# Kernel optimization log

Measured on AMD Instinct MI355X. Metric: run time of the kernel, lower is better.

## Reference

```python
import jax, jax.numpy as jnp
import numpy as np
from jax import lax

EPS = 1e-5

def ste_sign(x):
    # forward-only module: plain sign is fine
    return jnp.sign(x)

def conv2d(x, w, pad):
    # x: NCHW, w: OIHW, stride 1
    return lax.conv_general_dilated(x, w, window_strides=(1, 1),
                                    padding=[(pad, pad), (pad, pad)],
                                    dimension_numbers=('NCHW', 'OIHW', 'NCHW'))

def maxpool2(x):
    # 2x2 max pool, stride 2, VALID (floor) -- matches nn.MaxPool2d(2,2)
    return lax.reduce_window(x, -jnp.inf, lax.max, (1, 1, 2, 2), (1, 1, 2, 2), 'VALID')

def batchnorm(x, gamma, beta):
    # training-mode BN: batch statistics over (N,H,W), biased variance
    mean = jnp.mean(x, axis=(0, 2, 3), keepdims=True)
    var = jnp.var(x, axis=(0, 2, 3), keepdims=True)
    xn = (x - mean) * lax.rsqrt(var + EPS)
    return xn * gamma[None, :, None, None] + beta[None, :, None, None]

def setup_inputs() -> dict:
    key = jax.random.key(0)
    ks = jax.random.split(key, 8)
    def he(k, shape):
        n = shape[2] * shape[3] * shape[0]
        return jax.random.normal(k, shape, jnp.float32) * np.sqrt(2.0 / n)
    x = jax.random.normal(ks[0], (4096, 1, 28, 28), jnp.float32)
    w0 = he(ks[1], (32, 1, 3, 3))
    w1 = he(ks[2], (32, 32, 3, 3))
    w2 = he(ks[3], (32, 32, 3, 3))
    g0 = jnp.ones((32,), jnp.float32); b0 = jnp.zeros((32,), jnp.float32)
    g1 = jnp.ones((32,), jnp.float32); b1 = jnp.zeros((32,), jnp.float32)
    g2 = jnp.ones((32,), jnp.float32); b2 = jnp.zeros((32,), jnp.float32)
    fw = jax.random.normal(ks[4], (10, 288), jnp.float32) * 0.01
    fb = jnp.zeros((10,), jnp.float32)
    return {"x": x, "w0": w0, "g0": g0, "b0": b0, "w1": w1, "g1": g1, "b1": b1,
            "w2": w2, "g2": g2, "b2": b2, "fw": fw, "fb": fb}

def reference(x, w0, g0, b0, w1, g1, b1, w2, g2, b2, fw, fb):
    # block0: fp conv -> pool -> bn (no act)
    h = batchnorm(maxpool2(conv2d(x, w0, 1)), g0, b0)          # [B,32,14,14]
    # block1: binary(1w1a) conv -> pool -> bn + maxpool(shortcut)
    o = batchnorm(maxpool2(conv2d(ste_sign(h), ste_sign(w1), 1)), g1, b1)
    h = o + maxpool2(h)                                         # [B,32,7,7]
    # block2
    o = batchnorm(maxpool2(conv2d(ste_sign(h), ste_sign(w2), 1)), g2, b2)
    h = o + maxpool2(h)                                         # [B,32,3,3]
    h = h.reshape(h.shape[0], -1)                                # [B,288]
    return h @ fw.T + fb                                         # [B,10]
```

## Files before the change

kernel.cpp:

```cpp
#include <hip/hip_runtime.h>
#include <stdint.h>

#define BATCH 4096

typedef float v16f __attribute__((ext_vector_type(16)));
typedef short v8s  __attribute__((ext_vector_type(8)));

__global__ __launch_bounds__(448) void k_conv0f(const float* __restrict__ x,
                                                const float* __restrict__ w0,
                                                const float* __restrict__ w1,
                                                const float* __restrict__ w2,
                                                uint16_t* __restrict__ w1f,
                                                uint16_t* __restrict__ w2f,
                                                double* __restrict__ part0,
                                                float* __restrict__ mg) {
    __shared__ float xs[960];
    __shared__ float wl[288];
    __shared__ double rs[448], rq[448];
    int n = blockIdx.x, t = threadIdx.x;

    if (n < 72 && t < 256) {
        int i = n * 256 + t;
        int ii = (i < 9216) ? i : i - 9216;
        const float* w = (i < 9216) ? w1 : w2;
        uint16_t* o = (i < 9216) ? w1f : w2f;
        int j = ii & 7, nn = (ii >> 3) & 31, q2 = (ii >> 8) & 1, kh = (ii >> 9) & 1, tp = ii >> 10;
        int cin = kh * 16 + q2 * 8 + j;
        float v = w[(nn * 32 + cin) * 9 + tp];
        o[ii] = (v > 0.f) ? 0x3F80 : ((v < 0.f) ? 0xBF80 : 0);
    }

    for (int i = t; i < 960; i += 448) xs[i] = 0.f;
    for (int i = t; i < 288; i += 448) wl[i] = w0[i];
    __syncthreads();
    for (int i = t; i < 784; i += 448) {
        int y = i / 28, xx = i - y * 28;
        xs[(y + 1) * 32 + xx + 1] = x[n * 784 + i];
    }
    __syncthreads();
    int c = t & 31, py = t >> 5;
    float wreg[9];
    #pragma unroll
    for (int i = 0; i < 9; ++i) wreg[i] = wl[c * 9 + i];
    const float4* X4 = (const float4*)xs;
    float4 cur0 = X4[(2 * py + 0) * 8];
    float4 cur1 = X4[(2 * py + 1) * 8];
    float4 cur2 = X4[(2 * py + 2) * 8];
    float4 cur3 = X4[(2 * py + 3) * 8];
    float* mrow = mg + (size_t)n * 6272;
    double s = 0.0, q = 0.0;
    #pragma unroll
    for (int k = 0; k < 7; ++k) {
        float4 n0 = X4[(2 * py + 0) * 8 + k + 1];
        float4 n1 = X4[(2 * py + 1) * 8 + k + 1];
        float4 n2 = X4[(2 * py + 2) * 8 + k + 1];
        float4 n3 = X4[(2 * py + 3) * 8 + k + 1];
        float a[4][6];
        a[0][0] = cur0.x; a[0][1] = cur0.y; a[0][2] = cur0.z; a[0][3] = cur0.w; a[0][4] = n0.x; a[0][5] = n0.y;
        a[1][0] = cur1.x; a[1][1] = cur1.y; a[1][2] = cur1.z; a[1][3] = cur1.w; a[1][4] = n1.x; a[1][5] = n1.y;
        a[2][0] = cur2.x; a[2][1] = cur2.y; a[2][2] = cur2.z; a[2][3] = cur2.w; a[2][4] = n2.x; a[2][5] = n2.y;
        a[3][0] = cur3.x; a[3][1] = cur3.y; a[3][2] = cur3.z; a[3][3] = cur3.w; a[3][4] = n3.x; a[3][5] = n3.y;
        #pragma unroll
        for (int e = 0; e < 2; ++e) {
            int base = 2 * e;
            float s00 = 0.f, s01 = 0.f, s10 = 0.f, s11 = 0.f;
            #pragma unroll
            for (int ky = 0; ky < 3; ++ky)
            #pragma unroll
            for (int kx = 0; kx < 3; ++kx) {
                float w = wreg[ky * 3 + kx];
                s00 = fmaf(a[ky][base + kx], w, s00);
                s01 = fmaf(a[ky][base + kx + 1], w, s01);
                s10 = fmaf(a[ky + 1][base + kx], w, s10);
                s11 = fmaf(a[ky + 1][base + kx + 1], w, s11);
            }
            float m = fmaxf(fmaxf(s00, s01), fmaxf(s10, s11));
            int pix = py * 14 + 2 * k + e;
            mrow[pix * 32 + c] = m;
            double v = (double)m;
            s += v; q += v * v;
        }
        cur0 = n0; cur1 = n1; cur2 = n2; cur3 = n3;
    }
    rs[c * 14 + py] = s; rq[c * 14 + py] = q;
    __syncthreads();
    if (t < 32) {
        double S = 0.0, Q = 0.0;
        #pragma unroll
        for (int i = 0; i < 14; ++i) { S += rs[t * 14 + i]; Q += rq[t * 14 + i]; }
        part0[(size_t)t * 4096 + n] = S;
        part0[(size_t)32 * 4096 + (size_t)t * 4096 + n] = Q;
    }
}

__global__ __launch_bounds__(256) void k_finalize(const double* __restrict__ part, int G,
                                                  const float* __restrict__ g,
                                                  const float* __restrict__ b,
                                                  double inv_count, float* __restrict__ ss) {
    int c = blockIdx.x, t = threadIdx.x;
    double s = 0.0, q = 0.0;
    for (int i = t; i < G; i += 256) {
        s += part[(size_t)c * G + i];
        q += part[(size_t)32 * G + (size_t)c * G + i];
    }
    #pragma unroll
    for (int o = 32; o > 0; o >>= 1) { s += __shfl_down(s, o); q += __shfl_down(q, o); }
    __shared__ double rs[4], rq[4];
    int w = t >> 6, l = t & 63;
    if (l == 0) { rs[w] = s; rq[w] = q; }
    __syncthreads();
    if (t == 0) {
        s = rs[0] + rs[1] + rs[2] + rs[3];
        q = rq[0] + rq[1] + rq[2] + rq[3];
        double mean = s * inv_count;
        double var = q * inv_count - mean * mean;
        double sc = (double)g[c] / sqrt(var + 1e-5);
        ss[c] = (float)sc;
        ss[32 + c] = (float)((double)b[c] - mean * sc);
    }
}

__global__ __launch_bounds__(256) void k_conv1s(const float* __restrict__ m,
                                                const float* __restrict__ ss,
                                                const uint16_t* __restrict__ w1f,
                                                float* __restrict__ p1,
                                                double* __restrict__ part1) {
    __shared__ uint32_t lds[8192];
    int t = threadIdx.x;
    int n0 = blockIdx.x * 2;
    int lane = t & 63, wv = t >> 6;
    int q = lane >> 5, ncol = lane & 31;
    v8s wfr[18];
    #pragma unroll
    for (int f = 0; f < 18; ++f)
        wfr[f] = *(const v8s*)(w1f + (f * 2 + q) * 256 + ncol * 8);

    uint4 z4; z4.x = z4.y = z4.z = z4.w = 0u;
    for (int i = t; i < 480; i += 256) {
        int img = (i >= 240) ? 1 : 0;
        int e2 = i - img * 240;
        int e = e2 >> 2, qd = e2 & 3;
        int yh, xh;
        if (e < 16)      { yh = 0;      xh = e; }
        else if (e < 32) { yh = 15;     xh = e - 16; }
        else if (e < 46) { yh = e - 31; xh = 0; }
        else             { yh = e - 45; xh = 15; }
        *(uint4*)&lds[img * 4096 + (yh * 16 + xh) * 16 + qd * 4] = z4;
    }
    int u = t >> 2, tq = t & 3;
    float sc8[8], sh8[8];
    #pragma unroll
    for (int j = 0; j < 8; ++j) { sc8[j] = ss[tq * 8 + j]; sh8[j] = ss[32 + tq * 8 + j]; }
    for (int pg = u; pg < 392; pg += 64) {
        int img = (pg >= 196) ? 1 : 0;
        int pl = pg - img * 196;
        int iy = pl / 14, ix = pl - iy * 14;
        int yy = iy + 1, xx2 = ix + 1;
        int p = yy * 16 + xx2;
        int psw = (xx2 & 3) ^ (yy & 3);
        int qd = tq ^ psw;
        const float4* mp = (const float4*)(m + ((size_t)(n0 + img) * 196 + pl) * 32 + tq * 8);
        float4 v0 = mp[0], v1 = mp[1];
        float h[8];
        h[0] = fmaf(sc8[0], v0.x, sh8[0]); h[1] = fmaf(sc8[1], v0.y, sh8[1]);
        h[2] = fmaf(sc8[2], v0.z, sh8[2]); h[3] = fmaf(sc8[3], v0.w, sh8[3]);
        h[4] = fmaf(sc8[4], v1.x, sh8[4]); h[5] = fmaf(sc8[5], v1.y, sh8[5]);
        h[6] = fmaf(sc8[6], v1.z, sh8[6]); h[7] = fmaf(sc8[7], v1.w, sh8[7]);
        uint32_t d[4];
        #pragma unroll
        for (int j = 0; j < 4; ++j) {
            float h0 = h[2 * j], h1 = h[2 * j + 1];
            uint32_t b0 = (h0 > 0.f) ? 0x3F80u : ((h0 < 0.f) ? 0xBF80u : 0u);
            uint32_t b1 = (h1 > 0.f) ? 0x3F80u : ((h1 < 0.f) ? 0xBF80u : 0u);
            d[j] = b0 | (b1 << 16);
        }
        uint4 v; v.x = d[0]; v.y = d[1]; v.z = d[2]; v.w = d[3];
        *(uint4*)&lds[img * 4096 + p * 16 + qd * 4] = v;
    }
    __syncthreads();

    int img = wv >> 1, wh = wv & 1;
    int n = n0 + img;
    int ibase = img * 4096;
    int mm = lane & 31;
    int quad = mm & 3, pwl = mm >> 2;
    int dy = quad >> 1, dx = quad & 1;
    double sAcc = 0.0, qAcc = 0.0;
    for (int tile = wh; tile < 7; tile += 2) {
        int pw = tile * 8 + pwl;
        int pwc = min(pw, 48);
        int py = pwc / 7, px = pwc - py * 7;
        int pbase = (2 * py + dy) * 16 + 2 * px + dx;
        v16f acc;
        #pragma unroll
        for (int i = 0; i < 16; ++i) acc[i] = 0.f;
        #pragma unroll
        for (int tp = 0; tp < 9; ++tp) {
            int p = pbase + (tp / 3) * 16 + (tp % 3);
            int psw = (p ^ (p >> 4)) & 3;
            #pragma unroll
            for (int kh = 0; kh < 2; ++kh) {
                int g = kh * 2 + q;
                int idx = ibase + p * 16 + ((g ^ psw) << 2);
                v8s a = *(const v8s*)&lds[idx];
                acc = __builtin_amdgcn_mfma_f32_32x32x16_bf16(a, wfr[tp * 2 + kh], acc, 0, 0, 0);
            }
        }
        #pragma unroll
        for (int g4 = 0; g4 < 4; ++g4) {
            float mx = fmaxf(fmaxf(acc[4 * g4], acc[4 * g4 + 1]),
                             fmaxf(acc[4 * g4 + 2], acc[4 * g4 + 3]));
            int pwo = tile * 8 + 2 * g4 + q;
            if (pwo < 49) {
                p1[((size_t)n * 49 + pwo) * 32 + ncol] = mx;
                double v = (double)mx;
                sAcc += v; qAcc += v * v;
            }
        }
    }
    __syncthreads();
    double* red = (double*)lds;
    red[(wv * 2 + q) * 32 + ncol] = sAcc;
    red[256 + (wv * 2 + q) * 32 + ncol] = qAcc;
    __syncthreads();
    if (t < 32) {
        double S = 0.0, Q = 0.0;
        #pragma unroll
        for (int i = 0; i < 8; ++i) { S += red[i * 32 + t]; Q += red[256 + i * 32 + t]; }
        part1[(size_t)t * 2048 + blockIdx.x] = S;
        part1[(size_t)32 * 2048 + (size_t)t * 2048 + blockIdx.x] = Q;
    }
}

__global__ __launch_bounds__(256) void k_bc2m(const float* __restrict__ p1,
                                              const float* __restrict__ m,
                                              const float* __restrict__ ss,
                                              const uint16_t* __restrict__ w2f,
                                              float* __restrict__ p2,
                                              float* __restrict__ hp1,
                                              double* __restrict__ part2) {
    __shared__ uint32_t lds[8192];
    __shared__ float Htmp[1568];
    int t = threadIdx.x;
    int n0 = blockIdx.x * 8;
    int lane = t & 63, wv = t >> 6;
    int q = lane >> 5, ncol = lane & 31;

    int cb = t & 7;
    float sc1v[4], sh1v[4], sc0v[4], sh0v[4];
    #pragma unroll
    for (int j = 0; j < 4; ++j) {
        sc1v[j] = ss[64 + cb * 4 + j]; sh1v[j] = ss[96 + cb * 4 + j];
        sc0v[j] = ss[cb * 4 + j];      sh0v[j] = ss[32 + cb * 4 + j];
    }
    int pw0 = t >> 3;
    int py0 = pw0 / 7, px0 = pw0 - py0 * 7;
    int mb0 = ((2 * py0) * 14 + 2 * px0) * 8 + cb;
    int pw1 = 32 + (t >> 3);
    int py1 = pw1 / 7, px1 = pw1 - py1 * 7;
    int mb1 = ((2 * py1) * 14 + 2 * px1) * 8 + cb;

    float4 pa, pb, a0, a1, a2, a3, b0_, b1_, b2_, b3_;
    {
        const float4* P4 = (const float4*)(p1 + (size_t)n0 * 1568);
        const float4* M4 = (const float4*)(m + (size_t)n0 * 6272);
        pa = P4[t];
        a0 = M4[mb0]; a1 = M4[mb0 + 8]; a2 = M4[mb0 + 112]; a3 = M4[mb0 + 120];
        if (t < 136) {
            pb = P4[256 + t];
            b0_ = M4[mb1]; b1_ = M4[mb1 + 8]; b2_ = M4[mb1 + 112]; b3_ = M4[mb1 + 120];
        }
    }

    float4* Ht4 = (float4*)Htmp;
    for (int img = 0; img < 8; ++img) {
        float4 npa, npb, na0, na1, na2, na3, nb0, nb1, nb2, nb3;
        if (img < 7) {
            const float4* P4 = (const float4*)(p1 + (size_t)(n0 + img + 1) * 1568);
            const float4* M4 = (const float4*)(m + (size_t)(n0 + img + 1) * 6272);
            npa = P4[t];
            na0 = M4[mb0]; na1 = M4[mb0 + 8]; na2 = M4[mb0 + 112]; na3 = M4[mb0 + 120];
            if (t < 136) {
                npb = P4[256 + t];
                nb0 = M4[mb1]; nb1 = M4[mb1 + 8]; nb2 = M4[mb1 + 112]; nb3 = M4[mb1 + 120];
            }
        }
        if (img) __syncthreads();
        {
            float mx0 = fmaxf(fmaxf(a0.x, a1.x), fmaxf(a2.x, a3.x));
            float mx1 = fmaxf(fmaxf(a0.y, a1.y), fmaxf(a2.y, a3.y));
            float mx2 = fmaxf(fmaxf(a0.z, a1.z), fmaxf(a2.z, a3.z));
            float mx3 = fmaxf(fmaxf(a0.w, a1.w), fmaxf(a2.w, a3.w));
            float mn0 = fminf(fminf(a0.x, a1.x), fminf(a2.x, a3.x));
            float mn1 = fminf(fminf(a0.y, a1.y), fminf(a2.y, a3.y));
            float mn2 = fminf(fminf(a0.z, a1.z), fminf(a2.z, a3.z));
            float mn3 = fminf(fminf(a0.w, a1.w), fminf(a2.w, a3.w));
            float s0 = (sc0v[0] > 0.f) ? mx0 : mn0;
            float s1 = (sc0v[1] > 0.f) ? mx1 : mn1;
            float s2 = (sc0v[2] > 0.f) ? mx2 : mn2;
            float s3 = (sc0v[3] > 0.f) ? mx3 : mn3;
            float4 hv;
            hv.x = fmaf(sc1v[0], pa.x, sh1v[0]) + fmaf(sc0v[0], s0, sh0v[0]);
            hv.y = fmaf(sc1v[1], pa.y, sh1v[1]) + fmaf(sc0v[1], s1, sh0v[1]);
            hv.z = fmaf(sc1v[2], pa.z, sh1v[2]) + fmaf(sc0v[2], s2, sh0v[2]);
            hv.w = fmaf(sc1v[3], pa.w, sh1v[3]) + fmaf(sc0v[3], s3, sh0v[3]);
            Ht4[t] = hv;
            if (t < 136) {
                float ux0 = fmaxf(fmaxf(b0_.x, b1_.x), fmaxf(b2_.x, b3_.x));
                float ux1 = fmaxf(fmaxf(b0_.y, b1_.y), fmaxf(b2_.y, b3_.y));
                float ux2 = fmaxf(fmaxf(b0_.z, b1_.z), fmaxf(b2_.z, b3_.z));
                float ux3 = fmaxf(fmaxf(b0_.w, b1_.w), fmaxf(b2_.w, b3_.w));
                float un0 = fminf(fminf(b0_.x, b1_.x), fminf(b2_.x, b3_.x));
                float un1 = fminf(fminf(b0_.y, b1_.y), fminf(b2_.y, b3_.y));
                float un2 = fminf(fminf(b0_.z, b1_.z), fminf(b2_.z, b3_.z));
                float un3 = fminf(fminf(b0_.w, b1_.w), fminf(b2_.w, b3_.w));
                float u0 = (sc0v[0] > 0.f) ? ux0 : un0;
                float u1 = (sc0v[1] > 0.f) ? ux1 : un1;
                float u2 = (sc0v[2] > 0.f) ? ux2 : un2;
                float u3 = (sc0v[3] > 0.f) ? ux3 : un3;
                float4 hw;
                hw.x = fmaf(sc1v[0], pb.x, sh1v[0]) + fmaf(sc0v[0], u0, sh0v[0]);
                hw.y = fmaf(sc1v[1], pb.y, sh1v[1]) + fmaf(sc0v[1], u1, sh0v[1]);
                hw.z = fmaf(sc1v[2], pb.z, sh1v[2]) + fmaf(sc0v[2], u2, sh0v[2]);
                hw.w = fmaf(sc1v[3], pb.w, sh1v[3]) + fmaf(sc0v[3], u3, sh0v[3]);
                Ht4[256 + t] = hw;
            }
        }
        __syncthreads();
        uint32_t* ap = &lds[img * 1024];
        #pragma unroll
        for (int ii = 0; ii < 4; ++ii) {
            int i = t + ii * 256;
            int pp = i >> 4, r = i & 15;
            int y = pp >> 3, xq = pp & 7;
            uint32_t d = 0u;
            if (y >= 1 && xq >= 1) {
                int pix = (y - 1) * 7 + (xq - 1);
                int sub = r & 3;
                int g = (r >> 2) ^ (pp & 3);
                int c0 = ((g << 2) | sub) * 2;
                float h0 = Htmp[pix * 32 + c0];
                float h1 = Htmp[pix * 32 + c0 + 1];
                uint32_t w0b = (h0 > 0.f) ? 0x3F80u : ((h0 < 0.f) ? 0xBF80u : 0u);
                uint32_t w1b = (h1 > 0.f) ? 0x3F80u : ((h1 < 0.f) ? 0xBF80u : 0u);
                d = w0b | (w1b << 16);
            }
            ap[i] = d;
        }
        for (int jj = t; jj < 288; jj += 256) {
            int c = jj / 9, pix = jj - c * 9;
            int r = pix / 3, qq = pix - r * 3;
            float e0 = Htmp[((2 * r) * 7 + 2 * qq) * 32 + c];
            float e1 = Htmp[((2 * r) * 7 + 2 * qq + 1) * 32 + c];
            float e2 = Htmp[((2 * r + 1) * 7 + 2 * qq) * 32 + c];
            float e3 = Htmp[((2 * r + 1) * 7 + 2 * qq + 1) * 32 + c];
            hp1[(size_t)(n0 + img) * 288 + c * 9 + pix] = fmaxf(fmaxf(e0, e1), fmaxf(e2, e3));
        }
        pa = npa; pb = npb;
        a0 = na0; a1 = na1; a2 = na2; a3 = na3;
        b0_ = nb0; b1_ = nb1; b2_ = nb2; b3_ = nb3;
    }
    __syncthreads();

    v8s wfr[18];
    #pragma unroll
    for (int f = 0; f < 18; ++f)
        wfr[f] = *(const v8s*)(w2f + (f * 2 + q) * 256 + ncol * 8);

    int mmm = lane & 31;
    int quad = mmm & 3, pwl = mmm >> 2;
    int dy = quad >> 1, dx = quad & 1;
    double sAcc = 0.0, qAcc = 0.0;
    for (int tile = wv; tile < 9; tile += 4) {
        int pwg = tile * 8 + pwl;
        int img = pwg / 9, pwi = pwg - img * 9;
        int py = pwi / 3, px = pwi - py * 3;
        int pbase = (2 * py + dy) * 8 + 2 * px + dx;
        v16f acc;
        #pragma unroll
        for (int i = 0; i < 16; ++i) acc[i] = 0.f;
        #pragma unroll
        for (int tp = 0; tp < 9; ++tp) {
            int p = pbase + (tp / 3) * 8 + (tp % 3);
            int psw = p & 3;
            #pragma unroll
            for (int kh = 0; kh < 2; ++kh) {
                int g = kh * 2 + q;
                int idx = img * 1024 + p * 16 + ((g ^ psw) << 2);
                v8s a = *(const v8s*)&lds[idx];
                acc = __builtin_amdgcn_mfma_f32_32x32x16_bf16(a, wfr[tp * 2 + kh], acc, 0, 0, 0);
            }
        }
        #pragma unroll
        for (int g4 = 0; g4 < 4; ++g4) {
            float mx = fmaxf(fmaxf(acc[4 * g4], acc[4 * g4 + 1]),
                             fmaxf(acc[4 * g4 + 2], acc[4 * g4 + 3]));
            int pwo = tile * 8 + 2 * g4 + q;
            int oimg = pwo / 9, opwi = pwo - oimg * 9;
            p2[(size_t)(n0 + oimg) * 288 + ncol * 9 + opwi] = mx;
            double v = (double)mx;
            sAcc += v; qAcc += v * v;
        }
    }
    __syncthreads();
    double* red = (double*)lds;
    red[(wv * 2 + q) * 32 + ncol] = sAcc;
    red[256 + (wv * 2 + q) * 32 + ncol] = qAcc;
    __syncthreads();
    if (t < 32) {
        double S = 0.0, Q = 0.0;
        #pragma unroll
        for (int i = 0; i < 8; ++i) { S += red[i * 32 + t]; Q += red[256 + i * 32 + t]; }
        part2[(size_t)t * 512 + blockIdx.x] = S;
        part2[(size_t)32 * 512 + (size_t)t * 512 + blockIdx.x] = Q;
    }
}

__global__ __launch_bounds__(256) void k_fc(const float* __restrict__ p2,
                                            const float* __restrict__ hp1,
                                            const float* __restrict__ ss,
                                            const float* __restrict__ fw,
                                            const float* __restrict__ fb,
                                            float* __restrict__ outv) {
    int wv = threadIdx.x >> 6, l = threadIdx.x & 63;
    int n = blockIdx.x * 4 + wv;
    float acc[10];
    #pragma unroll
    for (int k = 0; k < 10; ++k) acc[k] = 0.f;
    #pragma unroll
    for (int i = 0; i < 5; ++i) {
        int j = l + 64 * i;
        if (j < 288) {
            int c = j / 9;
            float h = fmaf(ss[128 + c], p2[n * 288 + j], ss[160 + c]) + hp1[n * 288 + j];
            #pragma unroll
            for (int k = 0; k < 10; ++k)
                acc[k] = fmaf(h, fw[k * 288 + j], acc[k]);
        }
    }
    #pragma unroll
    for (int k = 0; k < 10; ++k) {
        float s = acc[k];
        #pragma unroll
        for (int o = 32; o > 0; o >>= 1) s += __shfl_down(s, o);
        if (l == 0) outv[n * 10 + k] = s + fb[k];
    }
}

extern "C" void kernel_launch(void* const* d_in, const int* in_sizes, int n_in,
                              void* d_out, int out_size, void* d_ws, size_t ws_size,
                              hipStream_t stream) {
    (void)in_sizes; (void)n_in; (void)out_size; (void)ws_size;
    const float* x  = (const float*)d_in[0];
    const float* w0 = (const float*)d_in[1];
    const float* g0 = (const float*)d_in[2];
    const float* b0 = (const float*)d_in[3];
    const float* w1 = (const float*)d_in[4];
    const float* g1 = (const float*)d_in[5];
    const float* b1 = (const float*)d_in[6];
    const float* w2 = (const float*)d_in[7];
    const float* g2 = (const float*)d_in[8];
    const float* b2 = (const float*)d_in[9];
    const float* fw = (const float*)d_in[10];
    const float* fb = (const float*)d_in[11];
    float* outv = (float*)d_out;
    char* ws = (char*)d_ws;

    float*     ss    = (float*)(ws + 1024);
    uint16_t*  w1f   = (uint16_t*)(ws + 2048);
    uint16_t*  w2f   = (uint16_t*)(ws + 20480);
    double*    part1 = (double*)(ws + 38912);
    double*    part0 = (double*)(ws + 1087488);
    float*     p1    = (float*)(ws + 3184640);
    float*     p2    = (float*)(ws + 28874752);
    float*     hp1   = (float*)(ws + 33593344);
    double*    part2 = (double*)(ws + 38311936);
    float*     m     = (float*)(ws + 38574080);

    k_conv0f<<<BATCH, 448, 0, stream>>>(x, w0, w1, w2, w1f, w2f, part0, m);
    k_finalize<<<32, 256, 0, stream>>>(part0, 4096, g0, b0, 1.0 / (BATCH * 196.0), ss);

    k_conv1s<<<BATCH / 2, 256, 0, stream>>>(m, ss, w1f, p1, part1);
    k_finalize<<<32, 256, 0, stream>>>(part1, 2048, g1, b1, 1.0 / (BATCH * 49.0), ss + 64);

    k_bc2m<<<BATCH / 8, 256, 0, stream>>>(p1, m, ss, w2f, p2, hp1, part2);
    k_finalize<<<32, 256, 0, stream>>>(part2, 512, g2, b2, 1.0 / (BATCH * 9.0), ss + 128);

    k_fc<<<BATCH / 4, 256, 0, stream>>>(p2, hp1, ss, fw, fb, outv);
}
```

Baseline: 185.9 us.

## Give each wavefront its own images and LDS buffer in bc2m prologue

The prologue of the fused block1-epilogue/block2 kernel now assigns two images to each of the four wavefronts, each with a private LDS staging buffer. This replaces the block-wide loop over eight images that needed two __syncthreads per image. Only wave-local lgkmcnt waits and scheduling barriers remain. The trade-off is dropping the explicit register prefetch of the next image's global loads and growing LDS from 1568 to 6272 floats, which may lower occupancy.

```diff
diff --git a/kernel.cpp b/kernel.cpp
--- a/kernel.cpp
+++ b/kernel.cpp
@@ -240,53 +240,38 @@
                                               float* __restrict__ hp1,
                                               double* __restrict__ part2) {
     __shared__ uint32_t lds[8192];
-    __shared__ float Htmp[1568];
+    __shared__ float Hw[4][1568];
     int t = threadIdx.x;
     int n0 = blockIdx.x * 8;
     int lane = t & 63, wv = t >> 6;
     int q = lane >> 5, ncol = lane & 31;
 
-    int cb = t & 7;
+    int cq = lane & 7;
     float sc1v[4], sh1v[4], sc0v[4], sh0v[4];
     #pragma unroll
     for (int j = 0; j < 4; ++j) {
-        sc1v[j] = ss[64 + cb * 4 + j]; sh1v[j] = ss[96 + cb * 4 + j];
-        sc0v[j] = ss[cb * 4 + j];      sh0v[j] = ss[32 + cb * 4 + j];
-    }
-    int pw0 = t >> 3;
-    int py0 = pw0 / 7, px0 = pw0 - py0 * 7;
-    int mb0 = ((2 * py0) * 14 + 2 * px0) * 8 + cb;
-    int pw1 = 32 + (t >> 3);
-    int py1 = pw1 / 7, px1 = pw1 - py1 * 7;
-    int mb1 = ((2 * py1) * 14 + 2 * px1) * 8 + cb;
-
-    float4 pa, pb, a0, a1, a2, a3, b0_, b1_, b2_, b3_;
-    {
-        const float4* P4 = (const float4*)(p1 + (size_t)n0 * 1568);
-        const float4* M4 = (const float4*)(m + (size_t)n0 * 6272);
-        pa = P4[t];
-        a0 = M4[mb0]; a1 = M4[mb0 + 8]; a2 = M4[mb0 + 112]; a3 = M4[mb0 + 120];
-        if (t < 136) {
-            pb = P4[256 + t];
-            b0_ = M4[mb1]; b1_ = M4[mb1 + 8]; b2_ = M4[mb1 + 112]; b3_ = M4[mb1 + 120];
-        }
-    }
-
-    float4* Ht4 = (float4*)Htmp;
-    for (int img = 0; img < 8; ++img) {
-        float4 npa, npb, na0, na1, na2, na3, nb0, nb1, nb2, nb3;
-        if (img < 7) {
-            const float4* P4 = (const float4*)(p1 + (size_t)(n0 + img + 1) * 1568);
-            const float4* M4 = (const float4*)(m + (size_t)(n0 + img + 1) * 6272);
-            npa = P4[t];
-            na0 = M4[mb0]; na1 = M4[mb0 + 8]; na2 = M4[mb0 + 112]; na3 = M4[mb0 + 120];
-            if (t < 136) {
-                npb = P4[256 + t];
-                nb0 = M4[mb1]; nb1 = M4[mb1 + 8]; nb2 = M4[mb1 + 112]; nb3 = M4[mb1 + 120];
-            }
-        }
-        if (img) __syncthreads();
-        {
+        sc1v[j] = ss[64 + cq * 4 + j]; sh1v[j] = ss[96 + cq * 4 + j];
+        sc0v[j] = ss[cq * 4 + j];      sh0v[j] = ss[32 + cq * 4 + j];
+    }
+
+    float4* H4 = (float4*)Hw[wv];
+    float* Hp = Hw[wv];
+    #pragma unroll
+    for (int sIt = 0; sIt < 2; ++sIt) {
+        int img = 2 * wv + sIt;
+        int n = n0 + img;
+        const float4* P4 = (const float4*)(p1 + (size_t)n * 1568);
+        const float4* M4 = (const float4*)(m + (size_t)n * 6272);
+        if (sIt) {
+            asm volatile("s_waitcnt lgkmcnt(0)" ::: "memory");
+            __builtin_amdgcn_sched_barrier(0);
+        }
+        for (int e = lane; e < 392; e += 64) {
+            int pix = e >> 3;
+            int py = pix / 7, px = pix - py * 7;
+            int mb = ((2 * py) * 14 + 2 * px) * 8 + cq;
+            float4 a0 = M4[mb], a1 = M4[mb + 8], a2 = M4[mb + 112], a3 = M4[mb + 120];
+            float4 pv = P4[e];
             float mx0 = fmaxf(fmaxf(a0.x, a1.x), fmaxf(a2.x, a3.x));
             float mx1 = fmaxf(fmaxf(a0.y, a1.y), fmaxf(a2.y, a3.y));
             float mx2 = fmaxf(fmaxf(a0.z, a1.z), fmaxf(a2.z, a3.z));
@@ -300,37 +285,16 @@
             float s2 = (sc0v[2] > 0.f) ? mx2 : mn2;
             float s3 = (sc0v[3] > 0.f) ? mx3 : mn3;
             float4 hv;
-            hv.x = fmaf(sc1v[0], pa.x, sh1v[0]) + fmaf(sc0v[0], s0, sh0v[0]);
-            hv.y = fmaf(sc1v[1], pa.y, sh1v[1]) + fmaf(sc0v[1], s1, sh0v[1]);
-            hv.z = fmaf(sc1v[2], pa.z, sh1v[2]) + fmaf(sc0v[2], s2, sh0v[2]);
-            hv.w = fmaf(sc1v[3], pa.w, sh1v[3]) + fmaf(sc0v[3], s3, sh0v[3]);
-            Ht4[t] = hv;
-            if (t < 136) {
-                float ux0 = fmaxf(fmaxf(b0_.x, b1_.x), fmaxf(b2_.x, b3_.x));
-                float ux1 = fmaxf(fmaxf(b0_.y, b1_.y), fmaxf(b2_.y, b3_.y));
-                float ux2 = fmaxf(fmaxf(b0_.z, b1_.z), fmaxf(b2_.z, b3_.z));
-                float ux3 = fmaxf(fmaxf(b0_.w, b1_.w), fmaxf(b2_.w, b3_.w));
-                float un0 = fminf(fminf(b0_.x, b1_.x), fminf(b2_.x, b3_.x));
-                float un1 = fminf(fminf(b0_.y, b1_.y), fminf(b2_.y, b3_.y));
-                float un2 = fminf(fminf(b0_.z, b1_.z), fminf(b2_.z, b3_.z));
-                float un3 = fminf(fminf(b0_.w, b1_.w), fminf(b2_.w, b3_.w));
-                float u0 = (sc0v[0] > 0.f) ? ux0 : un0;
-                float u1 = (sc0v[1] > 0.f) ? ux1 : un1;
-                float u2 = (sc0v[2] > 0.f) ? ux2 : un2;
-                float u3 = (sc0v[3] > 0.f) ? ux3 : un3;
-                float4 hw;
-                hw.x = fmaf(sc1v[0], pb.x, sh1v[0]) + fmaf(sc0v[0], u0, sh0v[0]);
-                hw.y = fmaf(sc1v[1], pb.y, sh1v[1]) + fmaf(sc0v[1], u1, sh0v[1]);
-                hw.z = fmaf(sc1v[2], pb.z, sh1v[2]) + fmaf(sc0v[2], u2, sh0v[2]);
-                hw.w = fmaf(sc1v[3], pb.w, sh1v[3]) + fmaf(sc0v[3], u3, sh0v[3]);
-                Ht4[256 + t] = hw;
-            }
-        }
-        __syncthreads();
+            hv.x = fmaf(sc1v[0], pv.x, sh1v[0]) + fmaf(sc0v[0], s0, sh0v[0]);
+            hv.y = fmaf(sc1v[1], pv.y, sh1v[1]) + fmaf(sc0v[1], s1, sh0v[1]);
+            hv.z = fmaf(sc1v[2], pv.z, sh1v[2]) + fmaf(sc0v[2], s2, sh0v[2]);
+            hv.w = fmaf(sc1v[3], pv.w, sh1v[3]) + fmaf(sc0v[3], s3, sh0v[3]);
+            H4[e] = hv;
+        }
+        asm volatile("s_waitcnt lgkmcnt(0)" ::: "memory");
+        __builtin_amdgcn_sched_barrier(0);
         uint32_t* ap = &lds[img * 1024];
-        #pragma unroll
-        for (int ii = 0; ii < 4; ++ii) {
-            int i = t + ii * 256;
+        for (int i = lane; i < 1024; i += 64) {
             int pp = i >> 4, r = i & 15;
             int y = pp >> 3, xq = pp & 7;
             uint32_t d = 0u;
@@ -339,26 +303,23 @@
                 int sub = r & 3;
                 int g = (r >> 2) ^ (pp & 3);
                 int c0 = ((g << 2) | sub) * 2;
-                float h0 = Htmp[pix * 32 + c0];
-                float h1 = Htmp[pix * 32 + c0 + 1];
+                float h0 = Hp[pix * 32 + c0];
+                float h1 = Hp[pix * 32 + c0 + 1];
                 uint32_t w0b = (h0 > 0.f) ? 0x3F80u : ((h0 < 0.f) ? 0xBF80u : 0u);
                 uint32_t w1b = (h1 > 0.f) ? 0x3F80u : ((h1 < 0.f) ? 0xBF80u : 0u);
                 d = w0b | (w1b << 16);
             }
             ap[i] = d;
         }
-        for (int jj = t; jj < 288; jj += 256) {
+        for (int jj = lane; jj < 288; jj += 64) {
             int c = jj / 9, pix = jj - c * 9;
             int r = pix / 3, qq = pix - r * 3;
-            float e0 = Htmp[((2 * r) * 7 + 2 * qq) * 32 + c];
-            float e1 = Htmp[((2 * r) * 7 + 2 * qq + 1) * 32 + c];
-            float e2 = Htmp[((2 * r + 1) * 7 + 2 * qq) * 32 + c];
-            float e3 = Htmp[((2 * r + 1) * 7 + 2 * qq + 1) * 32 + c];
-            hp1[(size_t)(n0 + img) * 288 + c * 9 + pix] = fmaxf(fmaxf(e0, e1), fmaxf(e2, e3));
-        }
-        pa = npa; pb = npb;
-        a0 = na0; a1 = na1; a2 = na2; a3 = na3;
-        b0_ = nb0; b1_ = nb1; b2_ = nb2; b3_ = nb3;
+            float e0 = Hp[((2 * r) * 7 + 2 * qq) * 32 + c];
+            float e1 = Hp[((2 * r) * 7 + 2 * qq + 1) * 32 + c];
+            float e2 = Hp[((2 * r + 1) * 7 + 2 * qq) * 32 + c];
+            float e3 = Hp[((2 * r + 1) * 7 + 2 * qq + 1) * 32 + c];
+            hp1[(size_t)n * 288 + c * 9 + pix] = fmaxf(fmaxf(e0, e1), fmaxf(e2, e3));
+        }
     }
     __syncthreads();
 
```

Result: slower. 192.3 us (+3.4%).
